# Optimization experiments

Hardware: AMD Instinct MI355X
Metric: run time of the kernel (lower is better)

Reference implementation:

```python
import jax, jax.numpy as jnp
import numpy as np

NUM_CLASSES = 1000
MARGIN = 1.0
COS_EPS = 1e-8   # torch F.cosine_similarity eps
NORM_EPS = 1e-12 # torch F.normalize eps


def setup_inputs() -> dict:
    key = jax.random.key(0)
    k1, k2 = jax.random.split(key)
    N, D = 65536, 256
    embeddings = jax.random.normal(k1, (N, D), dtype=jnp.float32)
    labels = jax.random.randint(k2, (N,), 0, NUM_CLASSES)
    return {"embeddings": embeddings, "labels": labels}


def reference(embeddings, labels):
    N = embeddings.shape[0]
    # L2-normalize embeddings (torch F.normalize with eps clamp on norm)
    e_norm = jnp.maximum(jnp.linalg.norm(embeddings, axis=1, keepdims=True), NORM_EPS)
    e = embeddings / e_norm  # [N, D], unit rows

    # Per-class mean of normalized embeddings; zero vector for empty classes
    sums = jax.ops.segment_sum(e, labels, num_segments=NUM_CLASSES)          # [C, D]
    counts = jax.ops.segment_sum(jnp.ones((N,), e.dtype), labels,
                                 num_segments=NUM_CLASSES)                    # [C]
    centers = sums / jnp.maximum(counts, 1.0)[:, None]                        # [C, D]

    # cosine_similarity(e_i, center_j) = (e_i . c_j) / max(||e_i||*||c_j||, eps)
    # ||e_i|| == 1 (up to the normalize clamp), so denom = max(||c_j||, eps)
    c_norm = jnp.linalg.norm(centers, axis=1)                                 # [C]
    denom = jnp.maximum(c_norm, COS_EPS)
    sims = (e @ centers.T) / denom[None, :]                                   # [N, C]

    rows = jnp.arange(N)
    pos = jnp.square(sims[rows, labels] - 1.0)                                # [N]
    neg_all = jnp.square(jax.nn.relu(MARGIN - sims))                          # [N, C]
    neg_at_label = neg_all[rows, labels]                                      # [N]
    neg = (neg_all.sum(axis=1) - neg_at_label) / (NUM_CLASSES - 1)            # [N]

    return jnp.mean(pos + neg)
```

## Files before the change

### kernel.cpp

```cpp
#include <hip/hip_runtime.h>
#include <hip/hip_bf16.h>

#define NROWS 65536
#define DIM   256
#define NCLS  1000
#define CPAD  1024

typedef __attribute__((ext_vector_type(8))) short bf16x8;
typedef __attribute__((ext_vector_type(4))) float f32x4;

__device__ inline unsigned short f2bf(float x) {
    unsigned int u = __builtin_bit_cast(unsigned int, x);
    unsigned int lsb = (u >> 16) & 1u;
    u += 0x7fffu + lsb;
    return (unsigned short)(u >> 16);
}

__device__ inline float bf2f(unsigned short u) {
    unsigned int v = ((unsigned int)u) << 16;
    return __builtin_bit_cast(float, v);
}

__device__ inline void gload_lds16(const void* g, void* l) {
    __builtin_amdgcn_global_load_lds(
        (const __attribute__((address_space(1))) unsigned int*)g,
        (__attribute__((address_space(3))) unsigned int*)l, 16, 0, 0);
}

__global__ __launch_bounds__(256) void k_norm_acc(
    const float* __restrict__ emb, unsigned short* __restrict__ e,
    float* __restrict__ acc, unsigned int* __restrict__ done)
{
    int gid  = blockIdx.x * 256 + threadIdx.x;
    if (gid == 0) { *acc = 0.0f; *done = 0u; }
    int row  = gid >> 6;
    int lane = gid & 63;
    float4 v = ((const float4*)(emb + (size_t)row * DIM))[lane];
    float ss = v.x*v.x + v.y*v.y + v.z*v.z + v.w*v.w;
    #pragma unroll
    for (int off = 1; off < 64; off <<= 1) ss += __shfl_xor(ss, off);
    float inv = 1.0f / fmaxf(sqrtf(ss), 1e-12f);
    v.x *= inv; v.y *= inv; v.z *= inv; v.w *= inv;
    ushort4 u;
    u.x = f2bf(v.x); u.y = f2bf(v.y); u.z = f2bf(v.z); u.w = f2bf(v.w);
    ((ushort4*)(e + (size_t)row * DIM))[lane] = u;
}

__global__ __launch_bounds__(256) void k_gather_centers(
    const unsigned short* __restrict__ e, const int* __restrict__ labels,
    unsigned short* __restrict__ cs)
{
    const int c    = blockIdx.x;
    const int tid  = threadIdx.x;
    const int wave = tid >> 6, lane = tid & 63;

    if (c >= NCLS) {
        if (tid < 32) ((uint4*)(cs + (size_t)c * DIM))[tid] = make_uint4(0,0,0,0);
        return;
    }

    __shared__ float part[4][DIM];
    __shared__ unsigned int cnt_s[4];
    __shared__ float nred[4];

    float a0 = 0.f, a1 = 0.f, a2 = 0.f, a3 = 0.f;
    unsigned int cnt = 0;

    for (int it = 0; it < NROWS / 256 / 8; ++it) {
        int lb[8];
        #pragma unroll
        for (int u = 0; u < 8; ++u)
            lb[u] = labels[(it * 8 + u) * 256 + wave * 64 + lane];
        #pragma unroll
        for (int u = 0; u < 8; ++u) {
            unsigned long long m = __ballot(lb[u] == c);
            cnt += (unsigned int)__popcll(m);
            while (m) {
                int b = __ffsll((long long)m) - 1;
                m &= m - 1;
                int r = (it * 8 + u) * 256 + wave * 64 + b;
                ushort4 v = ((const ushort4*)(e + (size_t)r * DIM))[lane];
                a0 += bf2f(v.x); a1 += bf2f(v.y); a2 += bf2f(v.z); a3 += bf2f(v.w);
            }
        }
    }
    ((float4*)part[wave])[lane] = make_float4(a0, a1, a2, a3);
    if (lane == 0) cnt_s[wave] = cnt;
    __syncthreads();

    float s  = part[0][tid] + part[1][tid] + part[2][tid] + part[3][tid];
    float fc = (float)(cnt_s[0] + cnt_s[1] + cnt_s[2] + cnt_s[3]);
    float v  = s * (1.0f / fmaxf(fc, 1.0f));
    float vv = v * v;
    #pragma unroll
    for (int off = 32; off >= 1; off >>= 1) vv += __shfl_xor(vv, off);
    if (lane == 0) nred[wave] = vv;
    __syncthreads();
    float ss = nred[0] + nred[1] + nred[2] + nred[3];
    float sc = 1.0f / fmaxf(sqrtf(ss), 1e-8f);
    cs[(size_t)c * DIM + tid] = f2bf(v * sc);
}

#define TMB 128
#define TCB 128

__global__ __launch_bounds__(256, 2) void k_loss_mfma(
    const unsigned short* __restrict__ e, const unsigned short* __restrict__ cs,
    const int* __restrict__ labels, float* __restrict__ acc,
    unsigned int* __restrict__ done, float* __restrict__ out)
{
    __shared__ __align__(16) unsigned short a_s[2][TMB * 64];
    __shared__ __align__(16) unsigned short b_s[2][TCB * 64];
    __shared__ float red_s[4];

    const int tid  = threadIdx.x;
    const int row0 = blockIdx.x * TMB;
    const int wave = tid >> 6, lane = tid & 63;
    const int wm = wave >> 1, wn = wave & 1;
    const int l16 = lane & 15, q = lane >> 4;
    const int st_r = lane >> 3;
    const int st_s = (lane & 7) ^ st_r;

    int labv[16];
    #pragma unroll
    for (int mi = 0; mi < 4; ++mi)
        #pragma unroll
        for (int rg = 0; rg < 4; ++rg)
            labv[mi * 4 + rg] = labels[row0 + wm*64 + mi*16 + q*4 + rg];

    #pragma unroll
    for (int kc = 0; kc < 2; ++kc)
        #pragma unroll
        for (int ch = 0; ch < 4; ++ch) {
            int chunk = wave * 4 + ch;
            int row   = chunk * 8 + st_r;
            gload_lds16(&e[(size_t)(row0 + row) * DIM + kc * 64 + st_s * 8],
                        &a_s[kc][chunk * 512]);
        }
    bf16x8 af2[4][2], af3[4][2];
    #pragma unroll
    for (int mi = 0; mi < 4; ++mi) {
        const unsigned short* pa =
            e + (size_t)(row0 + wm*64 + mi*16 + l16) * DIM + 128 + q * 8;
        af2[mi][0] = *(const bf16x8*)pa;
        af2[mi][1] = *(const bf16x8*)(pa + 32);
        af3[mi][0] = *(const bf16x8*)(pa + 64);
        af3[mi][1] = *(const bf16x8*)(pa + 96);
    }
    #pragma unroll
    for (int ch = 0; ch < 4; ++ch) {
        int chunk = wave * 4 + ch;
        int row   = chunk * 8 + st_r;
        gload_lds16(&cs[(size_t)row * DIM + st_s * 8], &b_s[0][chunk * 512]);
    }
    __syncthreads();

    float la_bulk = 0.0f, la_corr = 0.0f;
    const float KN = 1.0f / 999.0f;

    for (int cb = 0; cb < CPAD / TCB; ++cb) {
        f32x4 accf[4][4];
        #pragma unroll
        for (int mi = 0; mi < 4; ++mi)
            #pragma unroll
            for (int ni = 0; ni < 4; ++ni)
                accf[mi][ni] = (f32x4){0.f, 0.f, 0.f, 0.f};

        #pragma unroll
        for (int kc = 0; kc < 4; ++kc) {
            if (cb < 7 || kc < 3) {
                const int cb2 = (kc == 3) ? cb + 1 : cb;
                const int kc2 = (kc + 1) & 3;
                #pragma unroll
                for (int ch = 0; ch < 4; ++ch) {
                    int chunk = wave * 4 + ch;
                    int row   = chunk * 8 + st_r;
                    gload_lds16(&cs[(size_t)(cb2 * TCB + row) * DIM + kc2 * 64 + st_s * 8],
                                &b_s[(kc + 1) & 1][chunk * 512]);
                }
            }
            const unsigned short* bs = b_s[kc & 1];
            #pragma unroll
            for (int kk = 0; kk < 2; ++kk) {
                bf16x8 af[4], bfr[4];
                #pragma unroll
                for (int mi = 0; mi < 4; ++mi) {
                    if (kc == 0 || kc == 1) {
                        int rowA = wm*64 + mi*16 + l16;
                        af[mi] = *(const bf16x8*)&a_s[kc][
                            rowA*64 + (((kk*4 + q) ^ (rowA & 7)) * 8)];
                    } else if (kc == 2) {
                        af[mi] = af2[mi][kk];
                    } else {
                        af[mi] = af3[mi][kk];
                    }
                }
                #pragma unroll
                for (int ni = 0; ni < 4; ++ni) {
                    int rowB = wn*64 + ni*16 + l16;
                    bfr[ni] = *(const bf16x8*)&bs[rowB*64 + (((kk*4 + q) ^ (rowB & 7)) * 8)];
                }
                #pragma unroll
                for (int mi = 0; mi < 4; ++mi)
                    #pragma unroll
                    for (int ni = 0; ni < 4; ++ni)
                        accf[mi][ni] = __builtin_amdgcn_mfma_f32_16x16x32_bf16(
                            af[mi], bfr[ni], accf[mi][ni], 0, 0, 0);
            }
            __syncthreads();
        }

        #pragma unroll
        for (int mi = 0; mi < 4; ++mi)
            #pragma unroll
            for (int rg = 0; rg < 4; ++rg) {
                #pragma unroll
                for (int ni = 0; ni < 4; ++ni) {
                    float t = 1.0f - accf[mi][ni][rg];
                    la_bulk += t * t;
                }
                int lr = labv[mi*4 + rg] - cb*128 - wn*64 - l16;
                if ((lr & ~48) == 0) {
                    int nih = lr >> 4;
                    float sv = (nih == 0) ? accf[mi][0][rg] :
                               (nih == 1) ? accf[mi][1][rg] :
                               (nih == 2) ? accf[mi][2][rg] : accf[mi][3][rg];
                    float t = 1.0f - sv;
                    la_corr += t * t;
                }
            }
    }

    float la = la_bulk * KN + la_corr * (1.0f - KN);
    #pragma unroll
    for (int off = 32; off >= 1; off >>= 1) la += __shfl_xor(la, off);
    if (lane == 0) red_s[wave] = la;
    __syncthreads();
    if (tid == 0) {
        atomicAdd(acc, red_s[0] + red_s[1] + red_s[2] + red_s[3]);
        __threadfence();
        unsigned int t = atomicAdd(done, 1u);
        if (t == (unsigned int)(NROWS / TMB) - 1u) {
            float v = atomicAdd(acc, 0.0f);
            out[0] = v * (1.0f / (float)NROWS) - 24.0f * (1.0f / 999.0f);
        }
    }
}

extern "C" void kernel_launch(void* const* d_in, const int* in_sizes, int n_in,
                              void* d_out, int out_size, void* d_ws, size_t ws_size,
                              hipStream_t stream)
{
    const float* emb    = (const float*)d_in[0];
    const int*   labels = (const int*)d_in[1];
    float*       out    = (float*)d_out;
    char*        ws     = (char*)d_ws;

    const size_t OFF_CS   = (size_t)NROWS * DIM * 2;
    const size_t OFF_ACC  = OFF_CS + (size_t)CPAD * DIM * 2;
    const size_t OFF_DONE = OFF_ACC + 16;

    unsigned short* e    = (unsigned short*)ws;
    unsigned short* cs   = (unsigned short*)(ws + OFF_CS);
    float*          acc  = (float*)(ws + OFF_ACC);
    unsigned int*   done = (unsigned int*)(ws + OFF_DONE);

    k_norm_acc      <<<NROWS / 4, 256, 0, stream>>>(emb, e, acc, done);
    k_gather_centers<<<CPAD, 256, 0, stream>>>(e, labels, cs);
    k_loss_mfma     <<<NROWS / TMB, 256, 0, stream>>>(e, cs, labels, acc, done, out);
}
```

Measured before the change: 172.1 us.

## Split center gather across two halves with atomics and add separate center-normalize kernel

The per-class gather now runs two blocks per class, each scanning half of the rows, and combines the partial sums and counts through global float atomics. A new small kernel turns the sums into normalized bf16 centers, and the padding classes come out as zero because their sums are cleared. The normalize kernel now handles 8 rows per wave with batched shuffle reductions and also zeroes the sums and counts buffers. The aim is to halve the serial label scan per block and get more blocks in flight, at the cost of an extra launch, atomic traffic and a non-deterministic float summation order.

```diff
diff --git a/kernel.cpp b/kernel.cpp
--- a/kernel.cpp
+++ b/kernel.cpp
@@ -29,57 +29,74 @@
 
 __global__ __launch_bounds__(256) void k_norm_acc(
     const float* __restrict__ emb, unsigned short* __restrict__ e,
+    float* __restrict__ sums, unsigned int* __restrict__ counts,
     float* __restrict__ acc, unsigned int* __restrict__ done)
 {
-    int gid  = blockIdx.x * 256 + threadIdx.x;
-    if (gid == 0) { *acc = 0.0f; *done = 0u; }
-    int row  = gid >> 6;
-    int lane = gid & 63;
-    float4 v = ((const float4*)(emb + (size_t)row * DIM))[lane];
-    float ss = v.x*v.x + v.y*v.y + v.z*v.z + v.w*v.w;
-    #pragma unroll
-    for (int off = 1; off < 64; off <<= 1) ss += __shfl_xor(ss, off);
-    float inv = 1.0f / fmaxf(sqrtf(ss), 1e-12f);
-    v.x *= inv; v.y *= inv; v.z *= inv; v.w *= inv;
-    ushort4 u;
-    u.x = f2bf(v.x); u.y = f2bf(v.y); u.z = f2bf(v.z); u.w = f2bf(v.w);
-    ((ushort4*)(e + (size_t)row * DIM))[lane] = u;
-}
-
-__global__ __launch_bounds__(256) void k_gather_centers(
+    const int tid = threadIdx.x;
+    const int bid = blockIdx.x;
+    if (tid < 128) sums[bid * 128 + tid] = 0.0f;
+    if (bid < 16 && tid < 64) counts[bid * 64 + tid] = 0u;
+    if (bid == 0 && tid == 0) { *acc = 0.0f; *done = 0u; }
+
+    const int wave = tid >> 6, lane = tid & 63;
+    const int w = bid * 4 + wave;
+
+    #pragma unroll
+    for (int i = 0; i < 2; ++i) {
+        const int rbase = w * 8 + i * 4;
+        float4 v[4];
+        #pragma unroll
+        for (int r = 0; r < 4; ++r)
+            v[r] = ((const float4*)(emb + (size_t)(rbase + r) * DIM))[lane];
+        float ss[4];
+        #pragma unroll
+        for (int r = 0; r < 4; ++r)
+            ss[r] = v[r].x*v[r].x + v[r].y*v[r].y + v[r].z*v[r].z + v[r].w*v[r].w;
+        #pragma unroll
+        for (int off = 1; off < 64; off <<= 1) {
+            #pragma unroll
+            for (int r = 0; r < 4; ++r) ss[r] += __shfl_xor(ss[r], off);
+        }
+        #pragma unroll
+        for (int r = 0; r < 4; ++r) {
+            float inv = 1.0f / fmaxf(sqrtf(ss[r]), 1e-12f);
+            ushort4 u;
+            u.x = f2bf(v[r].x * inv); u.y = f2bf(v[r].y * inv);
+            u.z = f2bf(v[r].z * inv); u.w = f2bf(v[r].w * inv);
+            ((ushort4*)(e + (size_t)(rbase + r) * DIM))[lane] = u;
+        }
+    }
+}
+
+__global__ __launch_bounds__(256) void k_gather_partial(
     const unsigned short* __restrict__ e, const int* __restrict__ labels,
-    unsigned short* __restrict__ cs)
-{
-    const int c    = blockIdx.x;
-    const int tid  = threadIdx.x;
+    float* __restrict__ sums, unsigned int* __restrict__ counts)
+{
+    const int c   = blockIdx.x >> 1;
+    const int h   = blockIdx.x & 1;
+    const int tid = threadIdx.x;
     const int wave = tid >> 6, lane = tid & 63;
-
-    if (c >= NCLS) {
-        if (tid < 32) ((uint4*)(cs + (size_t)c * DIM))[tid] = make_uint4(0,0,0,0);
-        return;
-    }
 
     __shared__ float part[4][DIM];
     __shared__ unsigned int cnt_s[4];
-    __shared__ float nred[4];
-
+
+    const int base = h * (NROWS / 2);
     float a0 = 0.f, a1 = 0.f, a2 = 0.f, a3 = 0.f;
     unsigned int cnt = 0;
 
-    for (int it = 0; it < NROWS / 256 / 8; ++it) {
+    for (int it = 0; it < (NROWS / 2) / 256 / 8; ++it) {
         int lb[8];
         #pragma unroll
         for (int u = 0; u < 8; ++u)
-            lb[u] = labels[(it * 8 + u) * 256 + wave * 64 + lane];
+            lb[u] = labels[base + (it * 8 + u) * 256 + wave * 64 + lane];
         #pragma unroll
         for (int u = 0; u < 8; ++u) {
             unsigned long long m = __ballot(lb[u] == c);
             cnt += (unsigned int)__popcll(m);
+            int rb = base + (it * 8 + u) * 256 + wave * 64;
             while (m) {
-                int b = __ffsll((long long)m) - 1;
-                m &= m - 1;
-                int r = (it * 8 + u) * 256 + wave * 64 + b;
-                ushort4 v = ((const ushort4*)(e + (size_t)r * DIM))[lane];
+                int b = __ffsll((long long)m) - 1;  m &= m - 1;
+                ushort4 v = ((const ushort4*)(e + (size_t)(rb + b) * DIM))[lane];
                 a0 += bf2f(v.x); a1 += bf2f(v.y); a2 += bf2f(v.z); a3 += bf2f(v.w);
             }
         }
@@ -88,17 +105,30 @@
     if (lane == 0) cnt_s[wave] = cnt;
     __syncthreads();
 
-    float s  = part[0][tid] + part[1][tid] + part[2][tid] + part[3][tid];
-    float fc = (float)(cnt_s[0] + cnt_s[1] + cnt_s[2] + cnt_s[3]);
-    float v  = s * (1.0f / fmaxf(fc, 1.0f));
-    float vv = v * v;
-    #pragma unroll
-    for (int off = 32; off >= 1; off >>= 1) vv += __shfl_xor(vv, off);
-    if (lane == 0) nred[wave] = vv;
-    __syncthreads();
-    float ss = nred[0] + nred[1] + nred[2] + nred[3];
+    float s = part[0][tid] + part[1][tid] + part[2][tid] + part[3][tid];
+    atomicAdd(&sums[(size_t)c * DIM + tid], s);
+    if (tid == 0)
+        atomicAdd(&counts[c], cnt_s[0] + cnt_s[1] + cnt_s[2] + cnt_s[3]);
+}
+
+__global__ __launch_bounds__(256) void k_centers(
+    const float* __restrict__ sums, const unsigned int* __restrict__ counts,
+    unsigned short* __restrict__ cs)
+{
+    int gid  = blockIdx.x * 256 + threadIdx.x;
+    int c    = gid >> 6;
+    int lane = gid & 63;
+    float4 v = ((const float4*)(sums + (size_t)c * DIM))[lane];
+    float ic = 1.0f / fmaxf((float)counts[c], 1.0f);
+    v.x *= ic; v.y *= ic; v.z *= ic; v.w *= ic;
+    float ss = v.x*v.x + v.y*v.y + v.z*v.z + v.w*v.w;
+    #pragma unroll
+    for (int off = 1; off < 64; off <<= 1) ss += __shfl_xor(ss, off);
     float sc = 1.0f / fmaxf(sqrtf(ss), 1e-8f);
-    cs[(size_t)c * DIM + tid] = f2bf(v * sc);
+    ushort4 u;
+    u.x = f2bf(v.x * sc); u.y = f2bf(v.y * sc);
+    u.z = f2bf(v.z * sc); u.w = f2bf(v.w * sc);
+    ((ushort4*)(cs + (size_t)c * DIM))[lane] = u;
 }
 
 #define TMB 128
@@ -257,15 +287,20 @@
     char*        ws     = (char*)d_ws;
 
     const size_t OFF_CS   = (size_t)NROWS * DIM * 2;
-    const size_t OFF_ACC  = OFF_CS + (size_t)CPAD * DIM * 2;
+    const size_t OFF_SUMS = OFF_CS + (size_t)CPAD * DIM * 2;
+    const size_t OFF_CNT  = OFF_SUMS + (size_t)CPAD * DIM * 4;
+    const size_t OFF_ACC  = OFF_CNT + (size_t)CPAD * 4;
     const size_t OFF_DONE = OFF_ACC + 16;
 
-    unsigned short* e    = (unsigned short*)ws;
-    unsigned short* cs   = (unsigned short*)(ws + OFF_CS);
-    float*          acc  = (float*)(ws + OFF_ACC);
-    unsigned int*   done = (unsigned int*)(ws + OFF_DONE);
-
-    k_norm_acc      <<<NROWS / 4, 256, 0, stream>>>(emb, e, acc, done);
-    k_gather_centers<<<CPAD, 256, 0, stream>>>(e, labels, cs);
+    unsigned short* e      = (unsigned short*)ws;
+    unsigned short* cs     = (unsigned short*)(ws + OFF_CS);
+    float*          sums   = (float*)(ws + OFF_SUMS);
+    unsigned int*   counts = (unsigned int*)(ws + OFF_CNT);
+    float*          acc    = (float*)(ws + OFF_ACC);
+    unsigned int*   done   = (unsigned int*)(ws + OFF_DONE);
+
+    k_norm_acc      <<<NROWS / 32, 256, 0, stream>>>(emb, e, sums, counts, acc, done);
+    k_gather_partial<<<NCLS * 2, 256, 0, stream>>>(e, labels, sums, counts);
+    k_centers       <<<CPAD / 4, 256, 0, stream>>>(sums, counts, cs);
     k_loss_mfma     <<<NROWS / TMB, 256, 0, stream>>>(e, cs, labels, acc, done, out);
 }
```

New measurement: 163.8 us. -4.8%, faster.

## Fuse row normalization into per-class gather and split classes across two halves

Applied to the files above, without the earlier changes.

Row normalization now happens inside the per-class gather kernel. Each block loads the raw fp32 rows for its class, normalizes them, writes the bf16 copy and accumulates the sum in fp32, so the separate normalize pass is gone. The work is split into two blocks per class, each covering half the rows, and a small new kernel adds the partial sums and normalizes the centers. This removes one full pass over the embeddings but makes the gather read fp32 rows, twice the bytes of bf16, and adds a third launch.

```diff
diff --git a/kernel.cpp b/kernel.cpp
--- a/kernel.cpp
+++ b/kernel.cpp
@@ -27,60 +27,49 @@
         (__attribute__((address_space(3))) unsigned int*)l, 16, 0, 0);
 }
 
-__global__ __launch_bounds__(256) void k_norm_acc(
-    const float* __restrict__ emb, unsigned short* __restrict__ e,
+__global__ __launch_bounds__(256) void k_gather_norm(
+    const float* __restrict__ emb, const int* __restrict__ labels,
+    unsigned short* __restrict__ e, float* __restrict__ sums_p,
+    unsigned int* __restrict__ counts_p,
     float* __restrict__ acc, unsigned int* __restrict__ done)
 {
-    int gid  = blockIdx.x * 256 + threadIdx.x;
-    if (gid == 0) { *acc = 0.0f; *done = 0u; }
-    int row  = gid >> 6;
-    int lane = gid & 63;
-    float4 v = ((const float4*)(emb + (size_t)row * DIM))[lane];
-    float ss = v.x*v.x + v.y*v.y + v.z*v.z + v.w*v.w;
-    #pragma unroll
-    for (int off = 1; off < 64; off <<= 1) ss += __shfl_xor(ss, off);
-    float inv = 1.0f / fmaxf(sqrtf(ss), 1e-12f);
-    v.x *= inv; v.y *= inv; v.z *= inv; v.w *= inv;
-    ushort4 u;
-    u.x = f2bf(v.x); u.y = f2bf(v.y); u.z = f2bf(v.z); u.w = f2bf(v.w);
-    ((ushort4*)(e + (size_t)row * DIM))[lane] = u;
-}
-
-__global__ __launch_bounds__(256) void k_gather_centers(
-    const unsigned short* __restrict__ e, const int* __restrict__ labels,
-    unsigned short* __restrict__ cs)
-{
-    const int c    = blockIdx.x;
-    const int tid  = threadIdx.x;
+    const int c   = blockIdx.x >> 1;
+    const int h   = blockIdx.x & 1;
+    const int tid = threadIdx.x;
     const int wave = tid >> 6, lane = tid & 63;
-
-    if (c >= NCLS) {
-        if (tid < 32) ((uint4*)(cs + (size_t)c * DIM))[tid] = make_uint4(0,0,0,0);
-        return;
-    }
+    if (blockIdx.x == 0 && tid == 0) { *acc = 0.0f; *done = 0u; }
 
     __shared__ float part[4][DIM];
     __shared__ unsigned int cnt_s[4];
-    __shared__ float nred[4];
-
+
+    const int base = h * (NROWS / 2);
     float a0 = 0.f, a1 = 0.f, a2 = 0.f, a3 = 0.f;
     unsigned int cnt = 0;
 
-    for (int it = 0; it < NROWS / 256 / 8; ++it) {
+    for (int it = 0; it < (NROWS / 2) / 256 / 8; ++it) {
         int lb[8];
         #pragma unroll
         for (int u = 0; u < 8; ++u)
-            lb[u] = labels[(it * 8 + u) * 256 + wave * 64 + lane];
+            lb[u] = labels[base + (it * 8 + u) * 256 + wave * 64 + lane];
         #pragma unroll
         for (int u = 0; u < 8; ++u) {
             unsigned long long m = __ballot(lb[u] == c);
             cnt += (unsigned int)__popcll(m);
+            int rb = base + (it * 8 + u) * 256 + wave * 64;
             while (m) {
-                int b = __ffsll((long long)m) - 1;
-                m &= m - 1;
-                int r = (it * 8 + u) * 256 + wave * 64 + b;
-                ushort4 v = ((const ushort4*)(e + (size_t)r * DIM))[lane];
-                a0 += bf2f(v.x); a1 += bf2f(v.y); a2 += bf2f(v.z); a3 += bf2f(v.w);
+                int b = __ffsll((long long)m) - 1;  m &= m - 1;
+                int r = rb + b;
+                float4 v = ((const float4*)(emb + (size_t)r * DIM))[lane];
+                float ss = v.x*v.x + v.y*v.y + v.z*v.z + v.w*v.w;
+                #pragma unroll
+                for (int off = 1; off < 64; off <<= 1) ss += __shfl_xor(ss, off);
+                float inv = 1.0f / fmaxf(sqrtf(ss), 1e-12f);
+                v.x *= inv; v.y *= inv; v.z *= inv; v.w *= inv;
+                ushort4 u16;
+                u16.x = f2bf(v.x); u16.y = f2bf(v.y);
+                u16.z = f2bf(v.z); u16.w = f2bf(v.w);
+                ((ushort4*)(e + (size_t)r * DIM))[lane] = u16;
+                a0 += v.x; a1 += v.y; a2 += v.z; a3 += v.w;
             }
         }
     }
@@ -88,17 +77,36 @@
     if (lane == 0) cnt_s[wave] = cnt;
     __syncthreads();
 
-    float s  = part[0][tid] + part[1][tid] + part[2][tid] + part[3][tid];
-    float fc = (float)(cnt_s[0] + cnt_s[1] + cnt_s[2] + cnt_s[3]);
-    float v  = s * (1.0f / fmaxf(fc, 1.0f));
-    float vv = v * v;
-    #pragma unroll
-    for (int off = 32; off >= 1; off >>= 1) vv += __shfl_xor(vv, off);
-    if (lane == 0) nred[wave] = vv;
-    __syncthreads();
-    float ss = nred[0] + nred[1] + nred[2] + nred[3];
-    float sc = 1.0f / fmaxf(sqrtf(ss), 1e-8f);
-    cs[(size_t)c * DIM + tid] = f2bf(v * sc);
+    float s = part[0][tid] + part[1][tid] + part[2][tid] + part[3][tid];
+    sums_p[((size_t)h * CPAD + c) * DIM + tid] = s;
+    if (tid == 0)
+        counts_p[h * CPAD + c] = cnt_s[0] + cnt_s[1] + cnt_s[2] + cnt_s[3];
+}
+
+__global__ __launch_bounds__(256) void k_centers(
+    const float* __restrict__ sums_p, const unsigned int* __restrict__ counts_p,
+    unsigned short* __restrict__ cs)
+{
+    int gid  = blockIdx.x * 256 + threadIdx.x;
+    int c    = gid >> 6;
+    int lane = gid & 63;
+    float4 v = make_float4(0.f, 0.f, 0.f, 0.f);
+    if (c < NCLS) {
+        float4 v0 = ((const float4*)(sums_p + ((size_t)0 * CPAD + c) * DIM))[lane];
+        float4 v1 = ((const float4*)(sums_p + ((size_t)1 * CPAD + c) * DIM))[lane];
+        v.x = v0.x + v1.x; v.y = v0.y + v1.y;
+        v.z = v0.z + v1.z; v.w = v0.w + v1.w;
+        float ic = 1.0f / fmaxf((float)(counts_p[c] + counts_p[CPAD + c]), 1.0f);
+        v.x *= ic; v.y *= ic; v.z *= ic; v.w *= ic;
+        float ss = v.x*v.x + v.y*v.y + v.z*v.z + v.w*v.w;
+        #pragma unroll
+        for (int off = 1; off < 64; off <<= 1) ss += __shfl_xor(ss, off);
+        float sc = 1.0f / fmaxf(sqrtf(ss), 1e-8f);
+        v.x *= sc; v.y *= sc; v.z *= sc; v.w *= sc;
+    }
+    ushort4 u;
+    u.x = f2bf(v.x); u.y = f2bf(v.y); u.z = f2bf(v.z); u.w = f2bf(v.w);
+    ((ushort4*)(cs + (size_t)c * DIM))[lane] = u;
 }
 
 #define TMB 128
@@ -257,15 +265,20 @@
     char*        ws     = (char*)d_ws;
 
     const size_t OFF_CS   = (size_t)NROWS * DIM * 2;
-    const size_t OFF_ACC  = OFF_CS + (size_t)CPAD * DIM * 2;
+    const size_t OFF_SUMS = OFF_CS + (size_t)CPAD * DIM * 2;
+    const size_t OFF_CNT  = OFF_SUMS + (size_t)2 * CPAD * DIM * 4;
+    const size_t OFF_ACC  = OFF_CNT + (size_t)2 * CPAD * 4;
     const size_t OFF_DONE = OFF_ACC + 16;
 
-    unsigned short* e    = (unsigned short*)ws;
-    unsigned short* cs   = (unsigned short*)(ws + OFF_CS);
-    float*          acc  = (float*)(ws + OFF_ACC);
-    unsigned int*   done = (unsigned int*)(ws + OFF_DONE);
-
-    k_norm_acc      <<<NROWS / 4, 256, 0, stream>>>(emb, e, acc, done);
-    k_gather_centers<<<CPAD, 256, 0, stream>>>(e, labels, cs);
-    k_loss_mfma     <<<NROWS / TMB, 256, 0, stream>>>(e, cs, labels, acc, done, out);
-}
+    unsigned short* e        = (unsigned short*)ws;
+    unsigned short* cs       = (unsigned short*)(ws + OFF_CS);
+    float*          sums_p   = (float*)(ws + OFF_SUMS);
+    unsigned int*   counts_p = (unsigned int*)(ws + OFF_CNT);
+    float*          acc      = (float*)(ws + OFF_ACC);
+    unsigned int*   done     = (unsigned int*)(ws + OFF_DONE);
+
+    k_gather_norm<<<NCLS * 2, 256, 0, stream>>>(emb, labels, e, sums_p,
+                                                counts_p, acc, done);
+    k_centers    <<<CPAD / 4, 256, 0, stream>>>(sums_p, counts_p, cs);
+    k_loss_mfma  <<<NROWS / TMB, 256, 0, stream>>>(e, cs, labels, acc, done, out);
+}
```

Result: no change. 171.1 us (-0.6%).
